# Kernel optimization log

Hardware: AMD Instinct MI355X
Metric: run time of the kernel (lower is better)

The kernel has to match this reference:

```python
import jax, jax.numpy as jnp
import numpy as np

DIM = 1024
HEADS = 16
D_HEAD = DIM // HEADS
SCALE = D_HEAD ** -0.5


def setup_inputs() -> dict:
    key = jax.random.key(0)
    k_x, k_qkv, k_out = jax.random.split(key, 3)
    x = jax.random.normal(k_x, (4, 2048, DIM), dtype=jnp.float32)
    # nn.Linear(dim, 3*dim, bias=False): weight shape [3*dim, dim], y = x @ W.T
    w_qkv = jax.random.normal(k_qkv, (3 * DIM, DIM), dtype=jnp.float32) * (DIM ** -0.5)
    w_out = jax.random.normal(k_out, (DIM, DIM), dtype=jnp.float32) * (DIM ** -0.5)
    return {"x": x, "w_qkv": w_qkv, "w_out": w_out}


def reference(x, w_qkv, w_out):
    b, n, _ = x.shape
    qkv = jnp.einsum('bnd,ed->bne', x, w_qkv)  # [b, n, 3*dim]
    q, k, v = jnp.split(qkv, 3, axis=-1)
    def to_heads(t):
        return t.reshape(b, n, HEADS, D_HEAD).transpose(0, 2, 1, 3)  # [b,h,n,d]
    q, k, v = to_heads(q), to_heads(k), to_heads(v)
    scores = jnp.einsum('bhqd,bhkd->bhqk', q, k) * SCALE  # [b,h,n,n]
    attn = jax.nn.softmax(scores, axis=-1)
    out = jnp.einsum('bhqk,bhkd->bhqd', attn, v)
    out = out.transpose(0, 2, 1, 3).reshape(b, n, DIM)
    return jnp.einsum('bnd,ed->bne', out, w_out)
```

## Files before the change

### kernel.cpp

```cpp
#include <hip/hip_runtime.h>
#include <hip/hip_bf16.h>
#include <math.h>


typedef __attribute__((ext_vector_type(8))) __bf16 bf16x8;
typedef __attribute__((ext_vector_type(4))) float f32x4;
typedef unsigned short u16;
typedef unsigned int u32;

#define SEQ   2048
#define BATCH 4
#define DIM_  1024
#define NH    16
#define DH    64
#define MTOK  8192
#define QSCALE 0.125f

typedef unsigned int __attribute__((address_space(1))) u32_as1;
typedef unsigned int __attribute__((address_space(3))) u32_as3;

__device__ __forceinline__ void async16(void* lds, const void* g) {
  __builtin_amdgcn_global_load_lds((const u32_as1*)g, (u32_as3*)lds, 16, 0, 0);
}

__device__ __forceinline__ u16 f2bf(float f) {
  union { float f; u32 u; } a; a.f = f;
  u32 u = a.u;
  u = u + 0x7fffu + ((u >> 16) & 1u);
  return (u16)(u >> 16);
}

__device__ __forceinline__ f32x4 mfma16(bf16x8 a, bf16x8 b, f32x4 c) {
  return __builtin_amdgcn_mfma_f32_16x16x32_bf16(a, b, c, 0, 0, 0);
}

__global__ void cast_kernel(const float* __restrict__ in, u16* __restrict__ out, int n4) {
  int i = blockIdx.x * blockDim.x + threadIdx.x;
  if (i >= n4) return;
  float4 v = ((const float4*)in)[i];
  ushort4 o;
  o.x = f2bf(v.x); o.y = f2bf(v.y); o.z = f2bf(v.z); o.w = f2bf(v.w);
  ((ushort4*)out)[i] = o;
}

template<int MODE>
__global__ __launch_bounds__(256)
void gemm_bt(const u16* __restrict__ A, const u16* __restrict__ Bm, int K,
             u16* __restrict__ oq, u16* __restrict__ ok, u16* __restrict__ ov,
             float* __restrict__ of) {
  __shared__ __align__(16) u16 As[128*32];
  __shared__ __align__(16) u16 Bs[128*32];
  const int tid = threadIdx.x;
  const int l = tid & 63;
  const int w = tid >> 6;
  const int wr = w >> 1, wc = w & 1;
  const int lr = l & 15, lg = l >> 4;
  const int bm = blockIdx.y, bn = blockIdx.x;

  f32x4 acc[4][4] = {};

  const int srow = w*16 + (l >> 2);
  const int scol = (l & 3) * 8;
  const u16* gA = A + (size_t)(bm*128 + srow) * K + scol;
  const u16* gB = Bm + (size_t)(bn*128 + srow) * K + scol;
  u16* lA0 = As + (w*16)*32;
  u16* lA1 = As + (w*16 + 64)*32;
  u16* lB0 = Bs + (w*16)*32;
  u16* lB1 = Bs + (w*16 + 64)*32;
  const size_t rstride = (size_t)64 * K;

  const int fA = (wr*64 + lr)*32 + lg*8;
  const int fB = (wc*64 + lr)*32 + lg*8;

  const int nk = K >> 5;
  for (int kk = 0; kk < nk; ++kk) {
    async16(lA0, gA);
    async16(lA1, gA + rstride);
    async16(lB0, gB);
    async16(lB1, gB + rstride);
    gA += 32; gB += 32;
    __syncthreads();
    bf16x8 af[4], bb[4];
#pragma unroll
    for (int m = 0; m < 4; ++m) af[m] = *(const bf16x8*)(As + fA + m*16*32);
#pragma unroll
    for (int n = 0; n < 4; ++n) bb[n] = *(const bf16x8*)(Bs + fB + n*16*32);
#pragma unroll
    for (int m = 0; m < 4; ++m)
#pragma unroll
      for (int n = 0; n < 4; ++n)
        acc[m][n] = mfma16(af[m], bb[n], acc[m][n]);
    __syncthreads();
  }

#pragma unroll
  for (int m = 0; m < 4; ++m) {
    const int row0 = bm*128 + wr*64 + m*16 + lg*4;
    const int b = row0 >> 11, nt0 = row0 & 2047;
#pragma unroll
    for (int n = 0; n < 4; ++n) {
      const int col = bn*128 + wc*64 + n*16 + lr;
      if (MODE == 1) {
#pragma unroll
        for (int r = 0; r < 4; ++r)
          of[(size_t)(row0 + r) * DIM_ + col] = acc[m][n][r];
      } else {
        const int which = col >> 10;
        const int rem = col & 1023;
        const int h = rem >> 6, d = rem & 63;
        if (which == 2) {
          u32 p0 = (u32)f2bf(acc[m][n][0]) | ((u32)f2bf(acc[m][n][1]) << 16);
          u32 p1 = (u32)f2bf(acc[m][n][2]) | ((u32)f2bf(acc[m][n][3]) << 16);
          uint2 val; val.x = p0; val.y = p1;
          *(uint2*)(ov + ((size_t)((b*NH + h)*DH + d)) * SEQ + nt0) = val;
        } else {
          u16* dst = (which == 0) ? oq : ok;
          const float sc = (which == 0) ? QSCALE : 1.f;
#pragma unroll
          for (int r = 0; r < 4; ++r)
            dst[((size_t)((b*NH + h)*SEQ + nt0 + r) << 6) + d] = f2bf(acc[m][n][r] * sc);
        }
      }
    }
  }
}

__global__ __launch_bounds__(256)
void attn_kernel(const u16* __restrict__ Q, const u16* __restrict__ Kk,
                 const u16* __restrict__ Vt, u16* __restrict__ Ao) {
  __shared__ __align__(16) u16 KsB[2][64*64];
  __shared__ __align__(16) u16 VsB[2][64*64];
  __shared__ __align__(16) u16 Pl[4*16*64];
  const int tid = threadIdx.x;
  const int l = tid & 63, w = tid >> 6;
  const int lr = l & 15, lg = l >> 4;
  const int bh = blockIdx.y;
  const int q0 = blockIdx.x * 64;
  const size_t base = (size_t)bh * SEQ * DH;

  bf16x8 aq0 = *(const bf16x8*)(Q + base + (size_t)(q0 + w*16 + lr)*DH + lg*8);
  bf16x8 aq1 = *(const bf16x8*)(Q + base + (size_t)(q0 + w*16 + lr)*DH + 32 + lg*8);

  float m_run[4], l_run[4];
  f32x4 o[4] = {};
#pragma unroll
  for (int r = 0; r < 4; ++r) { m_run[r] = -INFINITY; l_run[r] = 0.f; }

  const int srow = l >> 3;
  const int sch  = (l & 7) ^ srow;
  const u16* gK  = Kk + base + (size_t)(w*8 + srow)*DH + sch*8;
  const u16* gV  = Vt + base + (size_t)(w*8 + srow)*SEQ + sch*8;
  u16* Pw = Pl + w*16*64;

  const int NT = SEQ/64;
#define STAGE(bs, kt)                                            \
  do {                                                           \
    const u16* gKt_ = gK + (size_t)(kt)*64*DH;                   \
    async16(KsB[bs] + (w*8)*64, gKt_);                           \
    async16(KsB[bs] + (32 + w*8)*64, gKt_ + 32*DH);              \
    const u16* gVt_ = gV + (size_t)(kt)*64;                      \
    async16(VsB[bs] + (w*8)*64, gVt_);                           \
    async16(VsB[bs] + (32 + w*8)*64, gVt_ + (size_t)32*SEQ);     \
  } while (0)

  STAGE(0, 0);
  for (int kt = 0; kt < NT; ++kt) {
    const int cur = kt & 1;
    __syncthreads();
    if (kt + 1 < NT) STAGE(cur ^ 1, kt + 1);

    const u16* Ks = KsB[cur];
    const u16* Vs = VsB[cur];

    f32x4 s[4];
#pragma unroll
    for (int t = 0; t < 4; ++t) {
      const int row = t*16 + lr;
      const char* kb = (const char*)Ks + row*128;
      const int sw = (row & 7) << 4;
      bf16x8 b0 = *(const bf16x8*)(kb + ((lg*16) ^ sw));
      bf16x8 b1 = *(const bf16x8*)(kb + ((64 + lg*16) ^ sw));
      f32x4 sv = {};
      sv = mfma16(aq0, b0, sv);
      sv = mfma16(aq1, b1, sv);
      s[t] = sv;
    }

#pragma unroll
    for (int r = 0; r < 4; ++r) {
      float mm = fmaxf(fmaxf(s[0][r], s[1][r]), fmaxf(s[2][r], s[3][r]));
      mm = fmaxf(mm, __shfl_xor(mm, 1));
      mm = fmaxf(mm, __shfl_xor(mm, 2));
      mm = fmaxf(mm, __shfl_xor(mm, 4));
      mm = fmaxf(mm, __shfl_xor(mm, 8));
      const float mn = fmaxf(m_run[r], mm);
      const float sc_ = __expf(m_run[r] - mn);
      m_run[r] = mn;
      const int q = lg*4 + r;
      float su = 0.f;
#pragma unroll
      for (int t = 0; t < 4; ++t) {
        float pv = __expf(s[t][r] - mn);
        su += pv;
        const int k = t*16 + lr;
        *(u16*)((char*)Pw + q*128 + ((((k >> 3) ^ (q & 7)) << 4) | ((k & 7) << 1))) = f2bf(pv);
      }
      su += __shfl_xor(su, 1);
      su += __shfl_xor(su, 2);
      su += __shfl_xor(su, 4);
      su += __shfl_xor(su, 8);
      l_run[r] = l_run[r]*sc_ + su;
#pragma unroll
      for (int dt = 0; dt < 4; ++dt) o[dt][r] *= sc_;
    }

    const char* Pb = (const char*)Pw + lr*128;
    const int swp = (lr & 7) << 4;
    bf16x8 pa0 = *(const bf16x8*)(Pb + ((lg*16) ^ swp));
    bf16x8 pa1 = *(const bf16x8*)(Pb + ((64 + lg*16) ^ swp));
#pragma unroll
    for (int dt = 0; dt < 4; ++dt) {
      const int rowv = dt*16 + lr;
      const char* vb = (const char*)Vs + rowv*128;
      const int swv = (rowv & 7) << 4;
      bf16x8 bv0 = *(const bf16x8*)(vb + ((lg*16) ^ swv));
      bf16x8 bv1 = *(const bf16x8*)(vb + ((64 + lg*16) ^ swv));
      o[dt] = mfma16(pa0, bv0, o[dt]);
      o[dt] = mfma16(pa1, bv1, o[dt]);
    }
  }
#undef STAGE

  const int b = bh >> 4, h = bh & 15;
#pragma unroll
  for (int dt = 0; dt < 4; ++dt) {
#pragma unroll
    for (int r = 0; r < 4; ++r) {
      const int qq = q0 + w*16 + lg*4 + r;
      const int col = h*64 + dt*16 + lr;
      Ao[(size_t)(b*SEQ + qq)*DIM_ + col] = f2bf(o[dt][r] / l_run[r]);
    }
  }
}

extern "C" void kernel_launch(void* const* d_in, const int* in_sizes, int n_in,
                              void* d_out, int out_size, void* d_ws, size_t ws_size,
                              hipStream_t stream) {
  const float* x    = (const float*)d_in[0];
  const float* wqkv = (const float*)d_in[1];
  const float* wout = (const float*)d_in[2];
  float* out = (float*)d_out;
  char* ws = (char*)d_ws;

  u16* x_bf    = (u16*)(ws + 0);
  u16* wqkv_bf = (u16*)(ws + 16777216);
  u16* wout_bf = (u16*)(ws + 23068672);
  u16* q_bf    = (u16*)(ws + 25165824);
  u16* k_bf    = (u16*)(ws + 41943040);
  u16* vt_bf   = (u16*)(ws + 58720256);
  u16* a_bf    = (u16*)(ws + 75497472);

  cast_kernel<<<dim3(MTOK*DIM_/4/256), 256, 0, stream>>>(x, x_bf, MTOK*DIM_/4);
  cast_kernel<<<dim3(3*DIM_*DIM_/4/256), 256, 0, stream>>>(wqkv, wqkv_bf, 3*DIM_*DIM_/4);
  cast_kernel<<<dim3(DIM_*DIM_/4/256), 256, 0, stream>>>(wout, wout_bf, DIM_*DIM_/4);

  gemm_bt<0><<<dim3(3*DIM_/128, MTOK/128), 256, 0, stream>>>(
      x_bf, wqkv_bf, DIM_, q_bf, k_bf, vt_bf, nullptr);
  attn_kernel<<<dim3(SEQ/64, BATCH*NH), 256, 0, stream>>>(q_bf, k_bf, vt_bf, a_bf);
  gemm_bt<1><<<dim3(DIM_/128, MTOK/128), 256, 0, stream>>>(
      a_bf, wout_bf, DIM_, nullptr, nullptr, nullptr, out);
}
```

Baseline: 404.9 us.

## Use exp2 softmax with lazy rescaling and MFMA row sums in attention

Folds log2(e) into the Q scale so the softmax can use the hardware exp2 instead of expf. The running max is only updated, and O and l only rescaled, when some row's tile max exceeds the stored max by more than 8 (checked wave-wide with __any), which removes most per-tile rescales. Row sums now come from an MFMA of P against a ones vector instead of shuffle reductions, and P is packed to bf16 with v_cvt_pk_bf16_f32. The deferred max bounds P values by 2^8 before bf16 rounding, which changes numerics slightly, and the row sum is taken from the bf16-rounded P rather than fp32 values.

```diff
diff --git a/kernel.cpp b/kernel.cpp
--- a/kernel.cpp
+++ b/kernel.cpp
@@ -14,7 +14,7 @@
 #define NH    16
 #define DH    64
 #define MTOK  8192
-#define QSCALE 0.125f
+#define QSCALE_L2E 0.180336880f
 
 typedef unsigned int __attribute__((address_space(1))) u32_as1;
 typedef unsigned int __attribute__((address_space(3))) u32_as3;
@@ -28,6 +28,20 @@
   u32 u = a.u;
   u = u + 0x7fffu + ((u >> 16) & 1u);
   return (u16)(u >> 16);
+}
+
+__device__ __forceinline__ float fexp2(float x) {
+#if __has_builtin(__builtin_amdgcn_exp2f)
+  return __builtin_amdgcn_exp2f(x);
+#else
+  return exp2f(x);
+#endif
+}
+
+__device__ __forceinline__ u32 cvtpk(float lo, float hi) {
+  u32 r;
+  asm("v_cvt_pk_bf16_f32 %0, %1, %2" : "=v"(r) : "v"(lo), "v"(hi));
+  return r;
 }
 
 __device__ __forceinline__ f32x4 mfma16(bf16x8 a, bf16x8 b, f32x4 c) {
@@ -115,7 +129,7 @@
           *(uint2*)(ov + ((size_t)((b*NH + h)*DH + d)) * SEQ + nt0) = val;
         } else {
           u16* dst = (which == 0) ? oq : ok;
-          const float sc = (which == 0) ? QSCALE : 1.f;
+          const float sc = (which == 0) ? QSCALE_L2E : 1.f;
 #pragma unroll
           for (int r = 0; r < 4; ++r)
             dst[((size_t)((b*NH + h)*SEQ + nt0 + r) << 6) + d] = f2bf(acc[m][n][r] * sc);
@@ -141,6 +155,10 @@
   bf16x8 aq0 = *(const bf16x8*)(Q + base + (size_t)(q0 + w*16 + lr)*DH + lg*8);
   bf16x8 aq1 = *(const bf16x8*)(Q + base + (size_t)(q0 + w*16 + lr)*DH + 32 + lg*8);
 
+  bf16x8 ones;
+#pragma unroll
+  for (int j = 0; j < 8; ++j) ones[j] = (__bf16)1.0f;
+
   float m_run[4], l_run[4];
   f32x4 o[4] = {};
 #pragma unroll
@@ -186,38 +204,58 @@
       s[t] = sv;
     }
 
+    float mm[4];
+    bool need = false;
 #pragma unroll
     for (int r = 0; r < 4; ++r) {
-      float mm = fmaxf(fmaxf(s[0][r], s[1][r]), fmaxf(s[2][r], s[3][r]));
-      mm = fmaxf(mm, __shfl_xor(mm, 1));
-      mm = fmaxf(mm, __shfl_xor(mm, 2));
-      mm = fmaxf(mm, __shfl_xor(mm, 4));
-      mm = fmaxf(mm, __shfl_xor(mm, 8));
-      const float mn = fmaxf(m_run[r], mm);
-      const float sc_ = __expf(m_run[r] - mn);
-      m_run[r] = mn;
+      float v = fmaxf(fmaxf(s[0][r], s[1][r]), fmaxf(s[2][r], s[3][r]));
+      v = fmaxf(v, __shfl_xor(v, 1));
+      v = fmaxf(v, __shfl_xor(v, 2));
+      v = fmaxf(v, __shfl_xor(v, 4));
+      v = fmaxf(v, __shfl_xor(v, 8));
+      mm[r] = v;
+      need = need || (v > m_run[r] + 8.f);
+    }
+    if (__any(need)) {
+#pragma unroll
+      for (int r = 0; r < 4; ++r) {
+        const float mn = fmaxf(m_run[r], mm[r]);
+        const float sc_ = fexp2(m_run[r] - mn);
+        m_run[r] = mn;
+        l_run[r] *= sc_;
+#pragma unroll
+        for (int dt = 0; dt < 4; ++dt) o[dt][r] *= sc_;
+      }
+    }
+
+#pragma unroll
+    for (int r = 0; r < 4; ++r) {
       const int q = lg*4 + r;
-      float su = 0.f;
-#pragma unroll
-      for (int t = 0; t < 4; ++t) {
-        float pv = __expf(s[t][r] - mn);
-        su += pv;
-        const int k = t*16 + lr;
-        *(u16*)((char*)Pw + q*128 + ((((k >> 3) ^ (q & 7)) << 4) | ((k & 7) << 1))) = f2bf(pv);
-      }
-      su += __shfl_xor(su, 1);
-      su += __shfl_xor(su, 2);
-      su += __shfl_xor(su, 4);
-      su += __shfl_xor(su, 8);
-      l_run[r] = l_run[r]*sc_ + su;
-#pragma unroll
-      for (int dt = 0; dt < 4; ++dt) o[dt][r] *= sc_;
+      char* basep = (char*)Pw + q*128;
+      const int sq = q & 7;
+      const int h0 = lr >> 3, lo = (lr & 7) << 1;
+      float p0 = fexp2(s[0][r] - m_run[r]);
+      float p1 = fexp2(s[1][r] - m_run[r]);
+      float p2 = fexp2(s[2][r] - m_run[r]);
+      float p3 = fexp2(s[3][r] - m_run[r]);
+      u32 a01 = cvtpk(p0, p1);
+      u32 a23 = cvtpk(p2, p3);
+      *(u16*)(basep + ((((0 + h0) ^ sq) << 4) | lo)) = (u16)a01;
+      *(u16*)(basep + ((((2 + h0) ^ sq) << 4) | lo)) = (u16)(a01 >> 16);
+      *(u16*)(basep + ((((4 + h0) ^ sq) << 4) | lo)) = (u16)a23;
+      *(u16*)(basep + ((((6 + h0) ^ sq) << 4) | lo)) = (u16)(a23 >> 16);
     }
 
     const char* Pb = (const char*)Pw + lr*128;
     const int swp = (lr & 7) << 4;
     bf16x8 pa0 = *(const bf16x8*)(Pb + ((lg*16) ^ swp));
     bf16x8 pa1 = *(const bf16x8*)(Pb + ((64 + lg*16) ^ swp));
+    f32x4 osum = {};
+    osum = mfma16(pa0, ones, osum);
+    osum = mfma16(pa1, ones, osum);
+#pragma unroll
+    for (int r = 0; r < 4; ++r) l_run[r] += osum[r];
+
 #pragma unroll
     for (int dt = 0; dt < 4; ++dt) {
       const int rowv = dt*16 + lr;
```

After: 362.0 us. 1.12x faster.
